# Kernel optimization log

Hardware: AMD Instinct MI355X
Metric: run time of the kernel (lower is better)

## Reference

```python
import jax, jax.numpy as jnp
import numpy as np

B, C, T = 4, 512, 4096
N2 = 32          # d_state // 2 complex modes
H = 2048         # hidden_channels
EPS = 1e-5


def setup_inputs() -> dict:
    key = jax.random.key(0)
    ks = jax.random.split(key, 8)
    dt_min, dt_max = 1e-3, 1e-1
    log_dt = jax.random.uniform(ks[1], (C,)) * (np.log(dt_max) - np.log(dt_min)) + np.log(dt_min)
    return {
        "x": jax.random.normal(ks[0], (B, C, T), jnp.float32),
        # ChannelwiseLayerNorm affine params
        "gamma": jnp.ones((C,), jnp.float32),
        "beta": jnp.zeros((C,), jnp.float32),
        # S4D kernel params (standard S4D-Lin init)
        "log_dt": log_dt.astype(jnp.float32),
        "C_re": jax.random.normal(ks[2], (C, N2), jnp.float32),
        "C_im": jax.random.normal(ks[3], (C, N2), jnp.float32),
        "log_A_real": jnp.log(0.5 * jnp.ones((C, N2), jnp.float32)),
        "A_imag": jnp.tile(jnp.pi * jnp.arange(N2, dtype=jnp.float32), (C, 1)),
        "D": jax.random.normal(ks[4], (C,), jnp.float32),
        # S4D output linear (Conv1d k=1 -> 2C, then GLU over channels)
        "Wo": jax.random.normal(ks[5], (2 * C, C), jnp.float32) / np.sqrt(C),
        "bo": jnp.zeros((2 * C,), jnp.float32),
        # FC MLP: Linear(C->H), PReLU(H), Linear(H->C)
        "W1": jax.random.normal(ks[6], (H, C), jnp.float32) / np.sqrt(C),
        "b1": jnp.zeros((H,), jnp.float32),
        "prelu_a": 0.25 * jnp.ones((H,), jnp.float32),
        "W2": jax.random.normal(ks[7], (C, H), jnp.float32) / np.sqrt(H),
        "b2": jnp.zeros((C,), jnp.float32),
    }


def reference(x, gamma, beta, log_dt, C_re, C_im, log_A_real, A_imag, D,
              Wo, bo, W1, b1, prelu_a, W2, b2):
    # ---- ChannelwiseLayerNorm over the channel dim of [B, C, T] ----
    mean = jnp.mean(x, axis=1, keepdims=True)
    var = jnp.var(x, axis=1, keepdims=True)
    u = gamma[None, :, None] * (x - mean) * jax.lax.rsqrt(var + EPS) + beta[None, :, None]

    # ---- S4D: diagonal SSM kernel via Vandermonde, applied by FFT conv ----
    L = x.shape[-1]
    dt = jnp.exp(log_dt)[:, None]                       # [C, 1]
    A = -jnp.exp(log_A_real) + 1j * A_imag              # [C, N2] complex diag
    dtA = A * dt                                        # [C, N2]
    Cd = (C_re + 1j * C_im) * (jnp.exp(dtA) - 1.0) / A  # discretized C (ZOH)
    vand = jnp.exp(dtA[..., None] * jnp.arange(L, dtype=jnp.float32))  # [C, N2, L]
    K = 2.0 * jnp.einsum('hn,hnl->hl', Cd, vand).real   # [C, L]

    k_f = jnp.fft.rfft(K, n=2 * L)                      # [C, L+1]
    u_f = jnp.fft.rfft(u, n=2 * L)                      # [B, C, L+1]
    y = jnp.fft.irfft(u_f * k_f, n=2 * L)[..., :L]      # causal conv
    y = y + u * D[None, :, None]                        # skip connection
    y = jax.nn.gelu(y, approximate=False)
    # output linear (1x1 conv to 2C) + GLU over channel dim
    z = jnp.einsum('oc,bct->bot', Wo, y) + bo[None, :, None]
    y = z[:, :C] * jax.nn.sigmoid(z[:, C:])             # [B, C, T]

    # ---- FC MLP with PReLU (per hidden channel) ----
    y = y.transpose(0, 2, 1)                            # [B, T, C]
    h = y @ W1.T + b1                                   # [B, T, H]
    h = jnp.where(h >= 0, h, prelu_a * h)
    y = h @ W2.T + b2                                   # [B, T, C]

    return x + y.transpose(0, 2, 1)                     # residual, [B, C, T]
```

## Files before the change

### kernel.cpp

```cpp
#include <hip/hip_runtime.h>
#include <math.h>

#define BB 4
#define CC 512
#define TT 4096
#define NN2 32
#define HH 2048

typedef __bf16 bf8v __attribute__((ext_vector_type(8)));
typedef __bf16 bf4v __attribute__((ext_vector_type(4)));
typedef float  f4v  __attribute__((ext_vector_type(4)));
typedef unsigned short u16x8 __attribute__((ext_vector_type(8)));

__device__ __forceinline__ void gload16(const void* g, void* l){
  __builtin_amdgcn_global_load_lds(
      (const __attribute__((address_space(1))) unsigned int*)g,
      (__attribute__((address_space(3))) unsigned int*)l, 16, 0, 0);
}
__device__ __forceinline__ float fast_gelu(float v){
  float x2 = v*v;
  float x  = 0.7978845608f*v*fmaf(0.044715f, x2, 1.0f);
  float t  = __expf(2.0f*x);
  return v - v*__builtin_amdgcn_rcpf(1.0f + t);
}
__device__ __forceinline__ float fast_sigmoid(float g){
  return __builtin_amdgcn_rcpf(1.0f + __expf(-g));
}
__device__ __forceinline__ unsigned short bfbits(float v){
  __bf16 h = (__bf16)v;
  return __builtin_bit_cast(unsigned short, h);
}

__global__ __launch_bounds__(256) void ln_kernel(
    const float* __restrict__ x, const float* __restrict__ gamma,
    const float* __restrict__ beta, __bf16* __restrict__ u)
{
  int tile = blockIdx.x & 63;
  int b    = blockIdx.x >> 6;
  int tl = threadIdx.x & 15;
  int cg = threadIdx.x >> 4;
  const float4* xp = (const float4*)(x + (size_t)b*CC*TT + tile*64) + tl;
  float4 s = {0,0,0,0}, s2 = {0,0,0,0};
  #pragma unroll 4
  for (int c = cg*32; c < (cg+1)*32; ++c){
    float4 v = xp[(size_t)c*(TT/4)];
    s.x += v.x; s.y += v.y; s.z += v.z; s.w += v.w;
    s2.x = fmaf(v.x,v.x,s2.x); s2.y = fmaf(v.y,v.y,s2.y);
    s2.z = fmaf(v.z,v.z,s2.z); s2.w = fmaf(v.w,v.w,s2.w);
  }
  __shared__ float4 ls[16][16], ls2[16][16], mean_s[16], inv_s[16];
  ls[cg][tl] = s; ls2[cg][tl] = s2;
  __syncthreads();
  if (threadIdx.x < 16){
    float4 ss = {0,0,0,0}, ss2 = {0,0,0,0};
    #pragma unroll
    for (int g2 = 0; g2 < 16; ++g2){
      float4 a = ls[g2][threadIdx.x], b2 = ls2[g2][threadIdx.x];
      ss.x+=a.x; ss.y+=a.y; ss.z+=a.z; ss.w+=a.w;
      ss2.x+=b2.x; ss2.y+=b2.y; ss2.z+=b2.z; ss2.w+=b2.w;
    }
    float4 mn, iv;
    mn.x = ss.x*(1.f/CC); mn.y = ss.y*(1.f/CC); mn.z = ss.z*(1.f/CC); mn.w = ss.w*(1.f/CC);
    iv.x = rsqrtf(ss2.x*(1.f/CC) - mn.x*mn.x + 1e-5f);
    iv.y = rsqrtf(ss2.y*(1.f/CC) - mn.y*mn.y + 1e-5f);
    iv.z = rsqrtf(ss2.z*(1.f/CC) - mn.z*mn.z + 1e-5f);
    iv.w = rsqrtf(ss2.w*(1.f/CC) - mn.w*mn.w + 1e-5f);
    mean_s[threadIdx.x] = mn; inv_s[threadIdx.x] = iv;
  }
  __syncthreads();
  float4 mn = mean_s[tl], iv = inv_s[tl];
  __bf16* up = u + (size_t)b*CC*TT + tile*64 + tl*4;
  #pragma unroll 4
  for (int c = cg*32; c < (cg+1)*32; ++c){
    float4 v = xp[(size_t)c*(TT/4)];
    float gi = gamma[c], be = beta[c];
    bf4v o;
    o[0] = (__bf16)fmaf(gi*iv.x, v.x - mn.x, be);
    o[1] = (__bf16)fmaf(gi*iv.y, v.y - mn.y, be);
    o[2] = (__bf16)fmaf(gi*iv.z, v.z - mn.z, be);
    o[3] = (__bf16)fmaf(gi*iv.w, v.w - mn.w, be);
    *(bf4v*)&up[(size_t)c*TT] = o;
  }
}

__global__ __launch_bounds__(256) void build_mats(
    const float* __restrict__ log_dt, const float* __restrict__ C_re,
    const float* __restrict__ C_im, const float* __restrict__ log_A_real,
    const float* __restrict__ A_imag, const float* __restrict__ Dp,
    __bf16* __restrict__ Tt, __bf16* __restrict__ V, __bf16* __restrict__ B2)
{
  __shared__ float cpart[4][64][33];
  __shared__ float kk[4][65];
  const int wv = threadIdx.x >> 6, lane = threadIdx.x & 63;
  const int c = blockIdx.x*4 + wv;
  const int m = lane & 31;
  float dt = expf(log_dt[c]);
  float Ar = -expf(log_A_real[c*NN2+m]);
  float Ai = A_imag[c*NN2+m];
  float er = expf(Ar*dt);
  float sw_, cw_; sincosf(Ai*dt, &sw_, &cw_);
  float wre = er*cw_, wim = er*sw_;
  float nr = wre-1.f, ni = wim;
  float inv = 1.f/(Ar*Ar + Ai*Ai);
  float qr = (nr*Ar + ni*Ai)*inv;
  float qi = (ni*Ar - nr*Ai)*inv;
  float Cr = C_re[c*NN2+m], Ci = C_im[c*NN2+m];
  float okr =  2.f*(Cr*qr - Ci*qi);
  float oki = -2.f*(Cr*qi + Ci*qr);
  __bf16* Ttc = Tt + (size_t)c*4096;
  __bf16* Vc  = V  + (size_t)c*4096;
  __bf16* B2c = B2 + (size_t)c*4096;
  if (lane < 32){
    float pre = 1.f, pim = 0.f;
    for (int l = 0; l <= 64; ++l){
      if (l <= 63){
        Vc[(2*m)*64   + (63-l)] = (__bf16)pre;
        Vc[(2*m+1)*64 + (63-l)] = (__bf16)pim;
      }
      float cR = fmaf(okr, pre,  oki*pim);
      float cQ = fmaf(oki, pre, -okr*pim);
      if (l <= 63) cpart[wv][l][m] = cR;
      if (l >= 1){
        B2c[(l-1)*64 + 2*m]   = (__bf16)cR;
        B2c[(l-1)*64 + 2*m+1] = (__bf16)cQ;
      }
      float npre = wre*pre - wim*pim;
      float npim = wre*pim + wim*pre;
      pre = npre; pim = npim;
    }
  }
  __syncthreads();
  float s = 0.f;
  #pragma unroll
  for (int mm = 0; mm < 32; ++mm) s += cpart[wv][lane][mm];
  if (lane == 0) s += Dp[c];
  kk[wv][lane] = s;
  __syncthreads();
  const int n = lane;
  #pragma unroll
  for (int kb = 0; kb < 8; ++kb){
    u16x8 v;
    #pragma unroll
    for (int e = 0; e < 8; ++e){
      int k = kb*8 + e;
      v[e] = bfbits((n >= k) ? kk[wv][n-k] : 0.f);
    }
    *(u16x8*)&Ttc[n*64 + kb*8] = v;
  }
}

__global__ __launch_bounds__(128) void s4dm_kernel(
    const __bf16* __restrict__ u, const float* __restrict__ log_dt,
    const float* __restrict__ log_A_real, const float* __restrict__ A_imag,
    const __bf16* __restrict__ Tt, const __bf16* __restrict__ V,
    const __bf16* __restrict__ B2, __bf16* __restrict__ gout)
{
  __shared__ __align__(16) float gbuf[2][64][66];
  __shared__ __align__(16) unsigned short s0buf[2][64][72];
  const int wv = threadIdx.x >> 6, l = threadIdx.x & 63;
  const int lr = l & 15, q = l >> 4;
  const int seq = blockIdx.x*2 + wv;
  const int c = seq & (CC-1);
  const __bf16* Up  = u  + (size_t)seq*TT;
  const __bf16* Ttc = Tt + (size_t)c*4096;
  const __bf16* Vc  = V  + (size_t)c*4096;
  const __bf16* B2c = B2 + (size_t)c*4096;

  f4v acc[4][4];
  #pragma unroll
  for (int a=0;a<4;++a)
    #pragma unroll
    for (int b=0;b<4;++b)
      #pragma unroll
      for (int r=0;r<4;++r) acc[a][b][r] = 0.f;

  #pragma unroll
  for (int kw = 0; kw < 2; ++kw){
    bf8v af[4], bv[4];
    #pragma unroll
    for (int mt=0;mt<4;++mt)
      af[mt] = *(const bf8v*)(Up + (mt*16+lr)*64 + kw*32 + q*8);
    #pragma unroll
    for (int nt=0;nt<4;++nt)
      bv[nt] = *(const bf8v*)(Vc + (nt*16+lr)*64 + kw*32 + q*8);
    #pragma unroll
    for (int mt=0;mt<4;++mt)
      #pragma unroll
      for (int nt=0;nt<4;++nt)
        acc[mt][nt] = __builtin_amdgcn_mfma_f32_16x16x32_bf16(af[mt], bv[nt], acc[mt][nt], 0,0,0);
  }
  #pragma unroll
  for (int mt=0;mt<4;++mt)
    #pragma unroll
    for (int nt=0;nt<4;++nt)
      #pragma unroll
      for (int r=0;r<4;++r)
        gbuf[wv][mt*16 + q*4 + r][nt*16 + lr] = acc[mt][nt][r];
  __syncthreads();

  if (l < 32){
    const int m = l;
    float dt = expf(log_dt[c]);
    float Ar = -expf(log_A_real[c*NN2+m]);
    float Ai = A_imag[c*NN2+m];
    float er = expf(Ar*dt);
    float sw_, cw_; sincosf(Ai*dt, &sw_, &cw_);
    float wr_ = er*cw_, wi_ = er*sw_;
    #pragma unroll
    for (int sq2=0;sq2<6;++sq2){
      float a=wr_, b=wi_;
      wr_ = a*a - b*b; wi_ = 2.f*a*b;
    }
    float S0r=0.f, S0i=0.f;
    for (int j=0;j<64;++j){
      float gr = gbuf[wv][j][2*m], gi = gbuf[wv][j][2*m+1];
      s0buf[wv][j][2*m]   = bfbits(S0r);
      s0buf[wv][j][2*m+1] = bfbits(S0i);
      float nRe = fmaf(wr_, S0r, fmaf(-wi_, S0i, gr));
      float nIm = fmaf(wr_, S0i, fmaf( wi_, S0r, gi));
      S0r = nRe; S0i = nIm;
    }
  }
  __syncthreads();

  #pragma unroll
  for (int a=0;a<4;++a)
    #pragma unroll
    for (int b=0;b<4;++b)
      #pragma unroll
      for (int r=0;r<4;++r) acc[a][b][r] = 0.f;
  #pragma unroll
  for (int kw = 0; kw < 2; ++kw){
    bf8v af[4], bv[4];
    #pragma unroll
    for (int mt=0;mt<4;++mt)
      af[mt] = *(const bf8v*)(Up + (mt*16+lr)*64 + kw*32 + q*8);
    #pragma unroll
    for (int nt=0;nt<4;++nt)
      bv[nt] = *(const bf8v*)(Ttc + (nt*16+lr)*64 + kw*32 + q*8);
    #pragma unroll
    for (int mt=0;mt<4;++mt)
      #pragma unroll
      for (int nt=0;nt<4;++nt)
        acc[mt][nt] = __builtin_amdgcn_mfma_f32_16x16x32_bf16(af[mt], bv[nt], acc[mt][nt], 0,0,0);
  }
  #pragma unroll
  for (int kw = 0; kw < 2; ++kw){
    bf8v af[4], bv[4];
    #pragma unroll
    for (int mt=0;mt<4;++mt)
      af[mt] = *(const bf8v*)&s0buf[wv][mt*16+lr][kw*32 + q*8];
    #pragma unroll
    for (int nt=0;nt<4;++nt)
      bv[nt] = *(const bf8v*)(B2c + (nt*16+lr)*64 + kw*32 + q*8);
    #pragma unroll
    for (int mt=0;mt<4;++mt)
      #pragma unroll
      for (int nt=0;nt<4;++nt)
        acc[mt][nt] = __builtin_amdgcn_mfma_f32_16x16x32_bf16(af[mt], bv[nt], acc[mt][nt], 0,0,0);
  }
  __syncthreads();

  unsigned short (*ybuf)[72] = (unsigned short(*)[72])&gbuf[wv][0][0];
  #pragma unroll
  for (int mt=0;mt<4;++mt)
    #pragma unroll
    for (int nt=0;nt<4;++nt)
      #pragma unroll
      for (int r=0;r<4;++r)
        ybuf[mt*16 + q*4 + r][nt*16 + lr] = bfbits(fast_gelu(acc[mt][nt][r]));
  __syncthreads();
  u16x8* dst = (u16x8*)(gout + (size_t)seq*TT);
  for (int i = l; i < 512; i += 64){
    int row = i >> 3, cq = i & 7;
    dst[i] = *(const u16x8*)&ybuf[row][cq*8];
  }
}

__global__ __launch_bounds__(256) void tr_kernel(const __bf16* __restrict__ gin,
                                                 __bf16* __restrict__ gout)
{
  __shared__ __align__(16) unsigned short ts[64][72];
  int bt = blockIdx.x;
  int bc = blockIdx.y;
  int b  = blockIdx.z;
  int tid = threadIdx.x;
  const __bf16* gp = gin + ((size_t)b*CC + bc*64)*TT + (size_t)bt*64;
  for (int i = tid; i < 512; i += 256){
    int c = i >> 3, tq = i & 7;
    u16x8 v = *(const u16x8*)(gp + (size_t)c*TT + tq*8);
    #pragma unroll
    for (int s = 0; s < 8; ++s) ts[tq*8+s][c] = v[s];
  }
  __syncthreads();
  __bf16* op = gout + ((size_t)b*TT + bt*64)*CC + bc*64;
  for (int i = tid; i < 512; i += 256){
    int t = i >> 3, cq = i & 7;
    u16x8 v = *(const u16x8*)&ts[t][cq*8];
    *(u16x8*)(op + (size_t)t*CC + cq*8) = v;
  }
}

__global__ __launch_bounds__(256) void cvt_kernel(const float4* __restrict__ in,
                                                  bf4v* __restrict__ out, int n4)
{
  int i = blockIdx.x*256 + threadIdx.x;
  if (i < n4){
    float4 v = in[i];
    bf4v o; o[0]=(__bf16)v.x; o[1]=(__bf16)v.y; o[2]=(__bf16)v.z; o[3]=(__bf16)v.w;
    out[i] = o;
  }
}

template<int MODE>
__global__ __launch_bounds__(256) void mm_kernel(
    const __bf16* __restrict__ Aw, const __bf16* __restrict__ Bt,
    const float* __restrict__ bias, const float* __restrict__ aux,
    void* __restrict__ outp)
{
  constexpr int K  = (MODE==2) ? 2048 : 512;
  constexpr int NT = K/32;
  constexpr int LOGGM = (MODE==1) ? 4 : 2;
  constexpr int GM = 1 << LOGGM;
  constexpr int LPS = (MODE==0) ? 6 : 4;

  __shared__ __align__(16) __bf16 As[2*128*32];
  __shared__ __align__(16) __bf16 Bs[2*128*32];
  __shared__ __align__(16) __bf16 As2[(MODE==0)?2*128*32:8];

  const int bid = blockIdx.x;
  const int X = bid & 7, L = bid >> 3;
  const int m0 = (L & (GM-1)) * 128;
  const int n0 = (X*16 + (L >> LOGGM)) * 128;

  const int tid = threadIdx.x;
  const int l = tid & 63;
  const int lr = l & 15, kh = l >> 4;
  const int w = tid >> 6;
  const int wr = w >> 1, wc = w & 1;
  const int coff = (kh ^ ((lr ^ (lr >> 2)) & 3)) * 16;

  f4v acc[4][4];
  f4v acc2[(MODE==0)?4:1][(MODE==0)?4:1];
  #pragma unroll
  for (int a=0;a<4;++a)
    #pragma unroll
    for (int b=0;b<4;++b)
      #pragma unroll
      for (int r=0;r<4;++r) acc[a][b][r] = 0.f;
  if constexpr (MODE==0){
    #pragma unroll
    for (int a=0;a<4;++a)
      #pragma unroll
      for (int b=0;b<4;++b)
        #pragma unroll
        for (int r=0;r<4;++r) acc2[a][b][r] = 0.f;
  }

  const char* pA  = (const char*)Aw;
  const char* pA2 = (const char*)(Aw + (size_t)CC*K);
  const char* pB  = (const char*)Bt;

  auto stage = [&](int d, int kt){
    #pragma unroll
    for (int i=0;i<2;++i){
      int cch = i*256 + tid;
      int row = cch >> 2;
      int kb = ((cch & 3) ^ ((row ^ (row >> 2)) & 3)) * 16;
      gload16(pA + ((size_t)(m0+row)*K + kt*32)*2 + kb, (char*)As + d*8192 + cch*16);
      gload16(pB + ((size_t)(n0+row)*K + kt*32)*2 + kb, (char*)Bs + d*8192 + cch*16);
      if constexpr (MODE==0)
        gload16(pA2 + ((size_t)(m0+row)*K + kt*32)*2 + kb, (char*)As2 + d*8192 + cch*16);
    }
  };

  auto compute = [&](int d){
    bf8v af[4], bv4[4];
    #pragma unroll
    for (int mi=0;mi<4;++mi){
      int row = wr*64 + mi*16 + lr;
      af[mi] = *(const bf8v*)((const char*)As + d*8192 + row*64 + coff);
    }
    #pragma unroll
    for (int ni=0;ni<4;++ni){
      int row = wc*64 + ni*16 + lr;
      bv4[ni] = *(const bf8v*)((const char*)Bs + d*8192 + row*64 + coff);
    }
    if constexpr (MODE==0){
      bf8v af2[4];
      #pragma unroll
      for (int mi=0;mi<4;++mi){
        int row = wr*64 + mi*16 + lr;
        af2[mi] = *(const bf8v*)((const char*)As2 + d*8192 + row*64 + coff);
      }
      __builtin_amdgcn_s_setprio(1);
      #pragma unroll
      for (int mi=0;mi<4;++mi)
        #pragma unroll
        for (int ni=0;ni<4;++ni){
          acc [mi][ni] = __builtin_amdgcn_mfma_f32_16x16x32_bf16(af [mi], bv4[ni], acc [mi][ni], 0,0,0);
          acc2[mi][ni] = __builtin_amdgcn_mfma_f32_16x16x32_bf16(af2[mi], bv4[ni], acc2[mi][ni], 0,0,0);
        }
      __builtin_amdgcn_s_setprio(0);
    } else {
      __builtin_amdgcn_s_setprio(1);
      #pragma unroll
      for (int mi=0;mi<4;++mi)
        #pragma unroll
        for (int ni=0;ni<4;++ni)
          acc[mi][ni] = __builtin_amdgcn_mfma_f32_16x16x32_bf16(af[mi], bv4[ni], acc[mi][ni], 0,0,0);
      __builtin_amdgcn_s_setprio(0);
    }
  };

  stage(0, 0);
  #pragma unroll 1
  for (int kt = 0; kt < NT; ++kt){
    if (kt + 1 < NT){
      stage((kt+1)&1, kt+1);
      asm volatile("s_waitcnt vmcnt(%0)" :: "n"(LPS) : "memory");
    } else {
      asm volatile("s_waitcnt vmcnt(0)" ::: "memory");
    }
    __builtin_amdgcn_s_barrier();
    compute(kt & 1);
    __builtin_amdgcn_s_barrier();
  }

  if constexpr (MODE==0 || MODE==1){
    const int COUT = (MODE==0) ? CC : HH;
    __bf16* O = (__bf16*)outp;
    #pragma unroll
    for (int mi=0;mi<4;++mi){
      int m = m0 + wr*64 + mi*16 + kh*4;
      float4 bi = *(const float4*)&bias[m];
      float bia[4] = {bi.x, bi.y, bi.z, bi.w};
      float gta[4], paa[4];
      if constexpr (MODE==0){
        float4 bg = *(const float4*)&bias[CC + m];
        gta[0]=bg.x; gta[1]=bg.y; gta[2]=bg.z; gta[3]=bg.w;
      } else {
        float4 pa = *(const float4*)&aux[m];
        paa[0]=pa.x; paa[1]=pa.y; paa[2]=pa.z; paa[3]=pa.w;
      }
      #pragma unroll
      for (int ni=0;ni<4;++ni){
        int tok = n0 + wc*64 + ni*16 + lr;
        bf4v o;
        #pragma unroll
        for (int r=0;r<4;++r){
          float v = acc[mi][ni][r] + bia[r];
          if constexpr (MODE==0){
            float gate = acc2[mi][ni][r] + gta[r];
            v = v * fast_sigmoid(gate);
          } else {
            v = (v >= 0.f) ? v : paa[r]*v;
          }
          o[r] = (__bf16)v;
        }
        *(bf4v*)&O[(size_t)tok*COUT + m] = o;
      }
    }
  } else {
    float* O = (float*)outp;
    #pragma unroll
    for (int mi=0;mi<4;++mi){
      int chb = m0 + wr*64 + mi*16 + kh*4;
      float4 bi = *(const float4*)&bias[chb];
      float bia[4] = {bi.x, bi.y, bi.z, bi.w};
      #pragma unroll
      for (int ni=0;ni<4;++ni){
        int tok = n0 + wc*64 + ni*16 + lr;
        int b = tok >> 12, t = tok & 4095;
        size_t rb = ((size_t)(b*CC + chb))*TT + t;
        #pragma unroll
        for (int r=0;r<4;++r)
          O[rb + (size_t)r*TT] = acc[mi][ni][r] + bia[r] + aux[rb + (size_t)r*TT];
      }
    }
  }
}

extern "C" void kernel_launch(void* const* d_in, const int* in_sizes, int n_in,
                              void* d_out, int out_size, void* d_ws, size_t ws_size,
                              hipStream_t stream)
{
  const float* x          = (const float*)d_in[0];
  const float* gamma      = (const float*)d_in[1];
  const float* beta       = (const float*)d_in[2];
  const float* log_dt     = (const float*)d_in[3];
  const float* C_re       = (const float*)d_in[4];
  const float* C_im       = (const float*)d_in[5];
  const float* log_A_real = (const float*)d_in[6];
  const float* A_imag     = (const float*)d_in[7];
  const float* Dp         = (const float*)d_in[8];
  const float* Wo         = (const float*)d_in[9];
  const float* bo         = (const float*)d_in[10];
  const float* W1         = (const float*)d_in[11];
  const float* b1         = (const float*)d_in[12];
  const float* prelu_a    = (const float*)d_in[13];
  const float* W2         = (const float*)d_in[14];
  const float* b2         = (const float*)d_in[15];
  float* out = (float*)d_out;

  char* base = (char*)d_ws;
  const size_t SEGB = (size_t)BB*CC*TT*2;
  __bf16* u_bf  = (__bf16*)(base);
  __bf16* glu   = (__bf16*)(base);
  __bf16* g_cm  = (__bf16*)(base + SEGB);
  __bf16* g_tm  = (__bf16*)(base + 2*SEGB);
  __bf16* h     = (__bf16*)(base + SEGB);
  __bf16* Tt_all = (__bf16*)(base + 2*SEGB);
  __bf16* V_all  = Tt_all + (size_t)CC*4096;
  __bf16* B2_all = V_all  + (size_t)CC*4096;
  __bf16* Wo_bf = (__bf16*)(base + 5*SEGB);
  __bf16* W1_bf = Wo_bf + (size_t)2*CC*CC;
  __bf16* W2_bf = W1_bf + (size_t)HH*CC;

  cvt_kernel<<<dim3((2*CC*CC/4 + 255)/256), 256, 0, stream>>>((const float4*)Wo, (bf4v*)Wo_bf, 2*CC*CC/4);
  cvt_kernel<<<dim3((HH*CC/4 + 255)/256), 256, 0, stream>>>((const float4*)W1, (bf4v*)W1_bf, HH*CC/4);
  cvt_kernel<<<dim3((CC*HH/4 + 255)/256), 256, 0, stream>>>((const float4*)W2, (bf4v*)W2_bf, CC*HH/4);

  build_mats<<<dim3(CC/4), 256, 0, stream>>>(log_dt, C_re, C_im, log_A_real,
                                             A_imag, Dp, Tt_all, V_all, B2_all);
  ln_kernel<<<dim3(BB*(TT/64)), 256, 0, stream>>>(x, gamma, beta, u_bf);
  s4dm_kernel<<<dim3((BB*CC)/2), 128, 0, stream>>>(u_bf, log_dt, log_A_real, A_imag,
                                                   Tt_all, V_all, B2_all, g_cm);
  tr_kernel<<<dim3(TT/64, CC/64, BB), 256, 0, stream>>>(g_cm, g_tm);

  mm_kernel<0><<<dim3(4*128),  256, 0, stream>>>(Wo_bf, g_tm, bo, nullptr, (void*)glu);
  mm_kernel<1><<<dim3(16*128), 256, 0, stream>>>(W1_bf, glu, b1, prelu_a, (void*)h);
  mm_kernel<2><<<dim3(4*128),  256, 0, stream>>>(W2_bf, h, b2, x, (void*)out);
}
```

Before: 218.3 us.

## Replace double-buffered BK=32 GEMM loop with single-buffered BK=64 tiles

The GEMM main loop drops the double-buffered LDS staging with explicit vmcnt waits and uses a single buffer with a K tile of 64 and an 8-way XOR swizzle. Each iteration loads the tile, syncs, runs two MFMA sub-steps, then syncs again. This halves the number of barriers per K and raises the work done per sync. The cost is that global loads no longer overlap with compute, and the s_setprio hints are removed.

Result: faster. 210.0 us (-3.8%).

```diff
diff --git a/kernel.cpp b/kernel.cpp
--- a/kernel.cpp
+++ b/kernel.cpp
@@ -319,14 +319,13 @@
     void* __restrict__ outp)
 {
   constexpr int K  = (MODE==2) ? 2048 : 512;
-  constexpr int NT = K/32;
+  constexpr int NT = K/64;
   constexpr int LOGGM = (MODE==1) ? 4 : 2;
   constexpr int GM = 1 << LOGGM;
-  constexpr int LPS = (MODE==0) ? 6 : 4;
-
-  __shared__ __align__(16) __bf16 As[2*128*32];
-  __shared__ __align__(16) __bf16 Bs[2*128*32];
-  __shared__ __align__(16) __bf16 As2[(MODE==0)?2*128*32:8];
+
+  __shared__ __align__(16) __bf16 As[128*64];
+  __shared__ __align__(16) __bf16 Bs[128*64];
+  __shared__ __align__(16) __bf16 As2[(MODE==0)?128*64:8];
 
   const int bid = blockIdx.x;
   const int X = bid & 7, L = bid >> 3;
@@ -338,7 +337,7 @@
   const int lr = l & 15, kh = l >> 4;
   const int w = tid >> 6;
   const int wr = w >> 1, wc = w & 1;
-  const int coff = (kh ^ ((lr ^ (lr >> 2)) & 3)) * 16;
+  const int swk = lr & 7;
 
   f4v acc[4][4];
   f4v acc2[(MODE==0)?4:1][(MODE==0)?4:1];
@@ -361,70 +360,60 @@
   const char* pA2 = (const char*)(Aw + (size_t)CC*K);
   const char* pB  = (const char*)Bt;
 
-  auto stage = [&](int d, int kt){
-    #pragma unroll
-    for (int i=0;i<2;++i){
+  #pragma unroll 1
+  for (int kt = 0; kt < NT; ++kt){
+    #pragma unroll
+    for (int i = 0; i < 4; ++i){
       int cch = i*256 + tid;
-      int row = cch >> 2;
-      int kb = ((cch & 3) ^ ((row ^ (row >> 2)) & 3)) * 16;
-      gload16(pA + ((size_t)(m0+row)*K + kt*32)*2 + kb, (char*)As + d*8192 + cch*16);
-      gload16(pB + ((size_t)(n0+row)*K + kt*32)*2 + kb, (char*)Bs + d*8192 + cch*16);
+      int row = cch >> 3;
+      int pos = cch & 7;
+      int q   = pos ^ (row & 7);
+      size_t gof = ((size_t)(m0+row)*K + kt*64)*2 + q*16;
+      size_t gofB = ((size_t)(n0+row)*K + kt*64)*2 + q*16;
+      gload16(pA + gof,  (char*)As + cch*16);
+      gload16(pB + gofB, (char*)Bs + cch*16);
       if constexpr (MODE==0)
-        gload16(pA2 + ((size_t)(m0+row)*K + kt*32)*2 + kb, (char*)As2 + d*8192 + cch*16);
-    }
-  };
-
-  auto compute = [&](int d){
-    bf8v af[4], bv4[4];
-    #pragma unroll
-    for (int mi=0;mi<4;++mi){
-      int row = wr*64 + mi*16 + lr;
-      af[mi] = *(const bf8v*)((const char*)As + d*8192 + row*64 + coff);
-    }
-    #pragma unroll
-    for (int ni=0;ni<4;++ni){
-      int row = wc*64 + ni*16 + lr;
-      bv4[ni] = *(const bf8v*)((const char*)Bs + d*8192 + row*64 + coff);
-    }
-    if constexpr (MODE==0){
-      bf8v af2[4];
+        gload16(pA2 + gof, (char*)As2 + cch*16);
+    }
+    __syncthreads();
+
+    #pragma unroll
+    for (int kk2 = 0; kk2 < 2; ++kk2){
+      const int coff = ((kk2*4 + kh) ^ swk) * 16;
+      bf8v af[4], bv4[4];
       #pragma unroll
       for (int mi=0;mi<4;++mi){
         int row = wr*64 + mi*16 + lr;
-        af2[mi] = *(const bf8v*)((const char*)As2 + d*8192 + row*64 + coff);
-      }
-      __builtin_amdgcn_s_setprio(1);
-      #pragma unroll
-      for (int mi=0;mi<4;++mi)
+        af[mi] = *(const bf8v*)((const char*)As + row*128 + coff);
+      }
+      #pragma unroll
+      for (int ni=0;ni<4;++ni){
+        int row = wc*64 + ni*16 + lr;
+        bv4[ni] = *(const bf8v*)((const char*)Bs + row*128 + coff);
+      }
+      if constexpr (MODE==0){
+        bf8v af2[4];
         #pragma unroll
-        for (int ni=0;ni<4;++ni){
-          acc [mi][ni] = __builtin_amdgcn_mfma_f32_16x16x32_bf16(af [mi], bv4[ni], acc [mi][ni], 0,0,0);
-          acc2[mi][ni] = __builtin_amdgcn_mfma_f32_16x16x32_bf16(af2[mi], bv4[ni], acc2[mi][ni], 0,0,0);
+        for (int mi=0;mi<4;++mi){
+          int row = wr*64 + mi*16 + lr;
+          af2[mi] = *(const bf8v*)((const char*)As2 + row*128 + coff);
         }
-      __builtin_amdgcn_s_setprio(0);
-    } else {
-      __builtin_amdgcn_s_setprio(1);
-      #pragma unroll
-      for (int mi=0;mi<4;++mi)
         #pragma unroll
-        for (int ni=0;ni<4;++ni)
-          acc[mi][ni] = __builtin_amdgcn_mfma_f32_16x16x32_bf16(af[mi], bv4[ni], acc[mi][ni], 0,0,0);
-      __builtin_amdgcn_s_setprio(0);
-    }
-  };
-
-  stage(0, 0);
-  #pragma unroll 1
-  for (int kt = 0; kt < NT; ++kt){
-    if (kt + 1 < NT){
-      stage((kt+1)&1, kt+1);
-      asm volatile("s_waitcnt vmcnt(%0)" :: "n"(LPS) : "memory");
-    } else {
-      asm volatile("s_waitcnt vmcnt(0)" ::: "memory");
-    }
-    __builtin_amdgcn_s_barrier();
-    compute(kt & 1);
-    __builtin_amdgcn_s_barrier();
+        for (int mi=0;mi<4;++mi)
+          #pragma unroll
+          for (int ni=0;ni<4;++ni){
+            acc [mi][ni] = __builtin_amdgcn_mfma_f32_16x16x32_bf16(af [mi], bv4[ni], acc [mi][ni], 0,0,0);
+            acc2[mi][ni] = __builtin_amdgcn_mfma_f32_16x16x32_bf16(af2[mi], bv4[ni], acc2[mi][ni], 0,0,0);
+          }
+      } else {
+        #pragma unroll
+        for (int mi=0;mi<4;++mi)
+          #pragma unroll
+          for (int ni=0;ni<4;++ni)
+            acc[mi][ni] = __builtin_amdgcn_mfma_f32_16x16x32_bf16(af[mi], bv4[ni], acc[mi][ni], 0,0,0);
+      }
+    }
+    __syncthreads();
   }
 
   if constexpr (MODE==0 || MODE==1){
```
